# Kernel tuning notes

Measured on AMD Instinct MI355X. Metric: run time of the kernel, lower is better.

The kernel has to match this reference:

```python
import jax, jax.numpy as jnp
import numpy as np

B, S, HID = 1, 2048, 2048
NH = 16
QL, KVL = 1536, 512
DN, DR, DV = 128, 64, 128
DQ = DN + DR  # 192
IH, ID = 4, 128
TOPK = 1024
EPS = 1e-6
THETA = 10000.0


def rope_interleaved(x, cos, sin):
    # x: (b,s,h,d); cos/sin: (s,d//2); pairs are (x[...,2i], x[...,2i+1])
    xr = x[..., 0::2]
    xi = x[..., 1::2]
    c = cos[None, :, None, :]
    s = sin[None, :, None, :]
    yr = xr * c - xi * s
    yi = xr * s + xi * c
    return jnp.stack([yr, yi], axis=-1).reshape(x.shape)


def rope_noninterleaved(x, cos, sin):
    # rotate-half style: pairs are (x[...,i], x[...,i+d/2])
    d = x.shape[-1] // 2
    x1, x2 = x[..., :d], x[..., d:]
    c = cos[None, :, None, :]
    s = sin[None, :, None, :]
    return jnp.concatenate([x1 * c - x2 * s, x1 * s + x2 * c], axis=-1)


def rmsnorm(x, w):
    var = jnp.mean(x * x, axis=-1, keepdims=True)
    return w * (x * jax.lax.rsqrt(var + EPS))


def layernorm(x, g, b):
    mu = jnp.mean(x, axis=-1, keepdims=True)
    var = jnp.mean((x - mu) ** 2, axis=-1, keepdims=True)
    return (x - mu) * jax.lax.rsqrt(var + EPS) * g + b


def setup_inputs() -> dict:
    key = jax.random.key(0)
    ks = jax.random.split(key, 12)
    std = 0.02
    x = jax.random.normal(ks[0], (B, S, HID), jnp.float32)
    pos = jnp.arange(S, dtype=jnp.float32)
    inv_freq = THETA ** (-jnp.arange(0, DR, 2, dtype=jnp.float32) / DR)
    ang = pos[:, None] * inv_freq[None, :]  # (S, DR//2)
    cos, sin = jnp.cos(ang), jnp.sin(ang)
    mask = jnp.where(jnp.tril(jnp.ones((S, S), bool)), 0.0, -1e9).astype(jnp.float32)
    return {
        "x": x, "cos": cos, "sin": sin, "mask": mask,
        "Wq_a": jax.random.normal(ks[1], (HID, QL), jnp.float32) * std,
        "q_norm_w": jnp.ones((QL,), jnp.float32),
        "Wq_b": jax.random.normal(ks[2], (QL, NH * DQ), jnp.float32) * std,
        "Wkv_a": jax.random.normal(ks[3], (HID, KVL + DR), jnp.float32) * std,
        "kv_norm_w": jnp.ones((KVL,), jnp.float32),
        "Wkv_b": jax.random.normal(ks[4], (KVL, NH * (DN + DV)), jnp.float32) * std,
        "Wo": jax.random.normal(ks[5], (NH * DV, HID), jnp.float32) * std,
        "IWq_b": jax.random.normal(ks[6], (QL, IH * ID), jnp.float32) * std,
        "IWk": jax.random.normal(ks[7], (HID, ID), jnp.float32) * std,
        "Ik_norm_w": jnp.ones((ID,), jnp.float32),
        "Ik_norm_b": jnp.zeros((ID,), jnp.float32),
        "IWproj": jax.random.normal(ks[8], (HID, IH), jnp.float32) * std,
    }


def indexer(x, qr, cos, sin, mask, IWq_b, IWk, Ik_norm_w, Ik_norm_b, IWproj):
    b, s, _ = x.shape
    q = (qr @ IWq_b).reshape(b, s, IH, ID)
    q_pe, q_nope = q[..., :DR], q[..., DR:]
    q_pe = rope_noninterleaved(q_pe, cos, sin)
    q = jnp.concatenate([q_pe, q_nope], axis=-1)
    k = layernorm(x @ IWk, Ik_norm_w, Ik_norm_b)  # (b,s,ID)
    k_pe = rope_noninterleaved(k[:, :, None, :DR], cos, sin)[:, :, 0]
    k = jnp.concatenate([k_pe, k[..., DR:]], axis=-1)
    weights = (x @ IWproj) * (IH ** -0.5) * (ID ** -0.5)  # (b,s,IH)
    logits = jax.nn.relu(jnp.einsum('bthd,bsd->btsh', q, k))
    index_score = jnp.einsum('btsh,bth->bts', logits, weights)
    index_score = index_score + mask[None]
    k_top = min(TOPK, s)
    topk_idx = jax.lax.top_k(index_score, k_top)[1]  # (b,s,k)
    bi = jnp.arange(b)[:, None, None]
    si = jnp.arange(s)[None, :, None]
    index_mask = jnp.full((b, s, s), -1e9, jnp.float32).at[bi, si, topk_idx].set(0.0)
    return index_mask


def reference(x, cos, sin, mask, Wq_a, q_norm_w, Wq_b, Wkv_a, kv_norm_w, Wkv_b, Wo,
              IWq_b, IWk, Ik_norm_w, Ik_norm_b, IWproj):
    b, s, _ = x.shape
    qr = rmsnorm(x @ Wq_a, q_norm_w)  # (b,s,QL)
    q = (qr @ Wq_b).reshape(b, s, NH, DQ)
    q_nope, q_pe = q[..., :DN], q[..., DN:]
    q_pe = rope_interleaved(q_pe, cos, sin)
    q = jnp.concatenate([q_nope, q_pe], axis=-1)
    kv_full = x @ Wkv_a
    kv, k_pe = kv_full[..., :KVL], kv_full[..., KVL:]
    kv = rmsnorm(kv, kv_norm_w)
    k_pe = rope_interleaved(k_pe[:, :, None, :], cos, sin)  # (b,s,1,DR)
    kv_exp = (kv @ Wkv_b).reshape(b, s, NH, DN + DV)
    k_nope, v = kv_exp[..., :DN], kv_exp[..., DN:]
    k = jnp.concatenate([k_nope, jnp.broadcast_to(k_pe, (b, s, NH, DR))], axis=-1)
    scores = jnp.einsum('bshd,bthd->bsht', q, k) * (DQ ** -0.5)
    index_mask = indexer(x, qr, cos, sin, mask, IWq_b, IWk, Ik_norm_w, Ik_norm_b, IWproj)
    scores = scores + index_mask[:, :, None, :] + mask[None, :, None, :]
    probs = jax.nn.softmax(scores, axis=-1)
    out = jnp.einsum('bsht,bthd->bshd', probs, v).reshape(b, s, NH * DV)
    return out @ Wo
```

## Files before the change

### kernel.cpp

```cpp
#include <hip/hip_runtime.h>
#include <math.h>
#include <stdint.h>

#define S 2048
#define HID 2048
#define NH 16
#define QL 1536
#define KVL 512
#define DN 128
#define DR 64
#define DV 128
#define DQ 192
#define IH 4
#define ID 128
#define TOPK 1024

#define N1 2244
#define N2 3584

#define CDIV(a,b) (((a)+(b)-1)/(b))

typedef float f32x4 __attribute__((ext_vector_type(4)));
typedef short bf16x8 __attribute__((ext_vector_type(8)));

__device__ __forceinline__ ushort f2b(float f) {
    uint32_t u = __float_as_uint(f);
    u += 0x7fffu + ((u >> 16) & 1u);
    return (ushort)(u >> 16);
}

#define GLL16(g, l)                                                            \
    __builtin_amdgcn_global_load_lds(                                          \
        (const __attribute__((address_space(1))) void*)(g),                    \
        (__attribute__((address_space(3))) void*)(l), 16, 0, 0)

__global__ __launch_bounds__(256) void gemm_bt(const ushort* __restrict__ A,
                                               const ushort* __restrict__ BT,
                                               float* __restrict__ C,
                                               int M, int N, int K) {
    __shared__ ushort As[128 * 32];
    __shared__ ushort Bs[128 * 32];
    const int tid = threadIdx.x;
    const int w = tid >> 6, l = tid & 63;
    const int quad = l >> 4, lane = l & 15;
    const int row0 = blockIdx.y * 128, col0 = blockIdx.x * 128;
    const int wr = (w >> 1) * 64, wc = (w & 1) * 64;
    f32x4 acc[4][4];
#pragma unroll
    for (int i = 0; i < 4; i++)
#pragma unroll
        for (int j = 0; j < 4; j++) acc[i][j] = (f32x4)0.f;

    const int srow = w * 32 + (l >> 2);
    const int c8 = (l & 3) * 8;
    const ushort* pa0 = A + (size_t)(row0 + srow) * K + c8;
    const ushort* pa1 = A + (size_t)(row0 + srow + 16) * K + c8;
    int bn0 = col0 + srow;      if (bn0 > N - 1) bn0 = N - 1;
    int bn1 = col0 + srow + 16; if (bn1 > N - 1) bn1 = N - 1;
    const ushort* pb0 = BT + (size_t)bn0 * K + c8;
    const ushort* pb1 = BT + (size_t)bn1 * K + c8;
    ushort* sa0 = As + srow * 32 + c8;
    ushort* sa1 = sa0 + 16 * 32;
    ushort* sb0 = Bs + srow * 32 + c8;
    ushort* sb1 = sb0 + 16 * 32;

    for (int k0 = 0; k0 < K; k0 += 32) {
        __syncthreads();
        GLL16(pa0 + k0, sa0);
        GLL16(pa1 + k0, sa1);
        GLL16(pb0 + k0, sb0);
        GLL16(pb1 + k0, sb1);
        __syncthreads();
        bf16x8 af[4], bf[4];
#pragma unroll
        for (int mi = 0; mi < 4; mi++)
            af[mi] = *(const bf16x8*)(As + (wr + mi * 16 + lane) * 32 + quad * 8);
#pragma unroll
        for (int ni = 0; ni < 4; ni++)
            bf[ni] = *(const bf16x8*)(Bs + (wc + ni * 16 + lane) * 32 + quad * 8);
#pragma unroll
        for (int mi = 0; mi < 4; mi++)
#pragma unroll
            for (int ni = 0; ni < 4; ni++)
                acc[mi][ni] = __builtin_amdgcn_mfma_f32_16x16x32_bf16(af[mi], bf[ni], acc[mi][ni], 0, 0, 0);
    }
#pragma unroll
    for (int mi = 0; mi < 4; mi++)
#pragma unroll
        for (int ni = 0; ni < 4; ni++)
#pragma unroll
            for (int r = 0; r < 4; r++) {
                int row = row0 + wr + mi * 16 + quad * 4 + r;
                int col = col0 + wc + ni * 16 + lane;
                if (col < N) C[(size_t)row * N + col] = acc[mi][ni][r];
            }
}

__global__ __launch_bounds__(256) void gemm_bt_h(const ushort* __restrict__ A,
                                                 const ushort* __restrict__ BT,
                                                 ushort* __restrict__ C,
                                                 int M, int N, int K) {
    __shared__ ushort As[128 * 32];
    __shared__ ushort Bs[128 * 32];
    const int tid = threadIdx.x;
    const int w = tid >> 6, l = tid & 63;
    const int quad = l >> 4, lane = l & 15;
    const int row0 = blockIdx.y * 128, col0 = blockIdx.x * 128;
    const int wr = (w >> 1) * 64, wc = (w & 1) * 64;
    f32x4 acc[4][4];
#pragma unroll
    for (int i = 0; i < 4; i++)
#pragma unroll
        for (int j = 0; j < 4; j++) acc[i][j] = (f32x4)0.f;

    const int srow = w * 32 + (l >> 2);
    const int c8 = (l & 3) * 8;
    const ushort* pa0 = A + (size_t)(row0 + srow) * K + c8;
    const ushort* pa1 = A + (size_t)(row0 + srow + 16) * K + c8;
    int bn0 = col0 + srow;      if (bn0 > N - 1) bn0 = N - 1;
    int bn1 = col0 + srow + 16; if (bn1 > N - 1) bn1 = N - 1;
    const ushort* pb0 = BT + (size_t)bn0 * K + c8;
    const ushort* pb1 = BT + (size_t)bn1 * K + c8;
    ushort* sa0 = As + srow * 32 + c8;
    ushort* sa1 = sa0 + 16 * 32;
    ushort* sb0 = Bs + srow * 32 + c8;
    ushort* sb1 = sb0 + 16 * 32;

    for (int k0 = 0; k0 < K; k0 += 32) {
        __syncthreads();
        GLL16(pa0 + k0, sa0);
        GLL16(pa1 + k0, sa1);
        GLL16(pb0 + k0, sb0);
        GLL16(pb1 + k0, sb1);
        __syncthreads();
        bf16x8 af[4], bf[4];
#pragma unroll
        for (int mi = 0; mi < 4; mi++)
            af[mi] = *(const bf16x8*)(As + (wr + mi * 16 + lane) * 32 + quad * 8);
#pragma unroll
        for (int ni = 0; ni < 4; ni++)
            bf[ni] = *(const bf16x8*)(Bs + (wc + ni * 16 + lane) * 32 + quad * 8);
#pragma unroll
        for (int mi = 0; mi < 4; mi++)
#pragma unroll
            for (int ni = 0; ni < 4; ni++)
                acc[mi][ni] = __builtin_amdgcn_mfma_f32_16x16x32_bf16(af[mi], bf[ni], acc[mi][ni], 0, 0, 0);
    }
#pragma unroll
    for (int mi = 0; mi < 4; mi++)
#pragma unroll
        for (int ni = 0; ni < 4; ni++)
#pragma unroll
            for (int r = 0; r < 4; r++) {
                int row = row0 + wr + mi * 16 + quad * 4 + r;
                int col = col0 + wc + ni * 16 + lane;
                if (col < N) C[(size_t)row * N + col] = f2b(acc[mi][ni][r]);
            }
}

__global__ __launch_bounds__(256) void wtrans(const float* __restrict__ W, ushort* __restrict__ WT,
                                              int K, int N) {
    __shared__ float t[64][65];
    int k0 = blockIdx.x * 64, n0 = blockIdx.y * 64;
    int rr = threadIdx.x >> 6, cc = threadIdx.x & 63;
#pragma unroll
    for (int p = 0; p < 16; p++) {
        int k = k0 + p * 4 + rr, n = n0 + cc;
        t[p * 4 + rr][cc] = (k < K && n < N) ? W[(size_t)k * N + n] : 0.f;
    }
    __syncthreads();
#pragma unroll
    for (int p = 0; p < 16; p++) {
        int n = n0 + p * 4 + rr, k = k0 + cc;
        if (n < N && k < K) WT[(size_t)n * K + k] = f2b(t[cc][p * 4 + rr]);
    }
}

__global__ void cvt_bf16(const float* __restrict__ in, ushort* __restrict__ out) {
    int i = blockIdx.x * 256 + threadIdx.x;
    float4 v = *(const float4*)(in + (size_t)i * 4);
    uint32_t lo = (uint32_t)f2b(v.x) | ((uint32_t)f2b(v.y) << 16);
    uint32_t hi = (uint32_t)f2b(v.z) | ((uint32_t)f2b(v.w) << 16);
    *(uint2*)(out + (size_t)i * 4) = make_uint2(lo, hi);
}

__global__ __launch_bounds__(256) void rmsnorm_b(const float* __restrict__ in, int istride,
                                                 ushort* __restrict__ out, int ostride,
                                                 const float* __restrict__ w, int L) {
    int row = blockIdx.x, tid = threadIdx.x;
    const float* xr = in + (size_t)row * istride;
    ushort* yr = out + (size_t)row * ostride;
    __shared__ float red[256];
    float ss = 0.f;
    for (int i = tid; i < L; i += 256) { float v = xr[i]; ss += v * v; }
    red[tid] = ss; __syncthreads();
    for (int st = 128; st > 0; st >>= 1) {
        if (tid < st) red[tid] += red[tid + st];
        __syncthreads();
    }
    float scale = rsqrtf(red[0] / (float)L + 1e-6f);
    for (int i = tid; i < L; i += 256) yr[i] = f2b(xr[i] * scale * w[i]);
}

__global__ void rope_q_b(const float* __restrict__ qf, ushort* __restrict__ qb,
                         const float* __restrict__ cosb, const float* __restrict__ sinb) {
    int idx = blockIdx.x * 256 + threadIdx.x;
    int p = idx % 96, h = (idx / 96) & 15, t = idx / (96 * 16);
    const float sc = 0.07216878364870322f;
    const float* src = qf + (size_t)t * N2 + h * 192;
    ushort* dst = qb + ((size_t)h * S + t) * 192;
    if (p < 64) {
        dst[2 * p]     = f2b(src[2 * p] * sc);
        dst[2 * p + 1] = f2b(src[2 * p + 1] * sc);
    } else {
        int j = p - 64;
        float c = cosb[t * 32 + j], s = sinb[t * 32 + j];
        float xr = src[128 + 2 * j], xi = src[128 + 2 * j + 1];
        dst[128 + 2 * j]     = f2b((xr * c - xi * s) * sc);
        dst[128 + 2 * j + 1] = f2b((xr * s + xi * c) * sc);
    }
}

__global__ void rope_kpe_kernel(const float* __restrict__ kvf, float* __restrict__ kpe,
                                const float* __restrict__ cosb, const float* __restrict__ sinb) {
    int idx = blockIdx.x * 256 + threadIdx.x;
    int j = idx & 31, t = idx >> 5;
    float c = cosb[t * 32 + j], s = sinb[t * 32 + j];
    const float* p = kvf + (size_t)t * N1 + 2 * j;
    float xr = p[0], xi = p[1];
    kpe[t * 64 + 2 * j] = xr * c - xi * s;
    kpe[t * 64 + 2 * j + 1] = xr * s + xi * c;
}

__global__ __launch_bounds__(256) void pack_kv(const ushort* __restrict__ kvexp_h,
                                               const float* __restrict__ kpe,
                                               ushort* __restrict__ kb,
                                               ushort* __restrict__ vT) {
    __shared__ ushort t[64][136];
    const int s0 = blockIdx.x * 64, h = blockIdx.y, tid = threadIdx.x;
    const int row = tid >> 2, c = tid & 3;
    const ushort* src = kvexp_h + (size_t)(s0 + row) * 4096 + h * 256;
    ushort* kbr = kb + ((size_t)h * S + s0 + row) * 192;
#pragma unroll
    for (int i = 0; i < 4; i++) {
        int off = c * 32 + i * 8;
        *(uint4*)(kbr + off) = *(const uint4*)(src + off);
        *(uint4*)(&t[row][off]) = *(const uint4*)(src + 128 + off);
    }
    const float* kp = kpe + (size_t)(s0 + row) * 64 + c * 16;
#pragma unroll
    for (int i = 0; i < 16; i++) kbr[128 + c * 16 + i] = f2b(kp[i]);
    __syncthreads();
    const int d = tid >> 1, sh = (tid & 1) * 32;
    ushort* dst = vT + ((size_t)h * 128 + d) * S + s0 + sh;
#pragma unroll
    for (int i = 0; i < 32; i++) dst[i] = t[sh + i][d];
}

__global__ void rope_qi_kernel(float* __restrict__ qi, const float* __restrict__ cosb,
                               const float* __restrict__ sinb) {
    int idx = blockIdx.x * 256 + threadIdx.x;
    int j = idx & 31, h = (idx >> 5) & 3, t = idx >> 7;
    float c = cosb[t * 32 + j], s = sinb[t * 32 + j];
    float* p = qi + (size_t)t * N2 + h * ID;
    float x1 = p[j], x2 = p[j + 32];
    p[j] = x1 * c - x2 * s;
    p[j + 32] = x1 * s + x2 * c;
}

__global__ __launch_bounds__(128) void ki_ln_rope_kernel(float* __restrict__ ki,
                                                         const float* __restrict__ g,
                                                         const float* __restrict__ bb,
                                                         const float* __restrict__ cosb,
                                                         const float* __restrict__ sinb) {
    int t = blockIdx.x, tid = threadIdx.x;
    float* p = ki + (size_t)t * N1;
    __shared__ float s1[128], s2m[128];
    float v = p[tid];
    s1[tid] = v; s2m[tid] = v * v; __syncthreads();
    for (int st = 64; st > 0; st >>= 1) {
        if (tid < st) { s1[tid] += s1[tid + st]; s2m[tid] += s2m[tid + st]; }
        __syncthreads();
    }
    float mu = s1[0] / 128.f;
    float var = s2m[0] / 128.f - mu * mu;
    float y = (v - mu) * rsqrtf(var + 1e-6f) * g[tid] + bb[tid];
    __syncthreads();
    s1[tid] = y; __syncthreads();
    if (tid >= 64) {
        p[tid] = y;
    } else if (tid < 32) {
        float c = cosb[t * 32 + tid], s = sinb[t * 32 + tid];
        float x1 = s1[tid], x2 = s1[tid + 32];
        p[tid] = x1 * c - x2 * s;
        p[tid + 32] = x1 * s + x2 * c;
    }
}

__global__ void transpose_ki_kernel(const float* __restrict__ ki, float* __restrict__ kiT) {
    int idx = blockIdx.x * 256 + threadIdx.x;
    int t = idx >> 7, d = idx & 127;
    kiT[(size_t)d * S + t] = ki[(size_t)t * N1 + d];
}

__global__ __launch_bounds__(256) void iscore4(const float* __restrict__ qi,
                                               const float* __restrict__ kiT,
                                               const float* __restrict__ iw,
                                               float* __restrict__ iscore) {
    int t = blockIdx.x;
    int s0 = blockIdx.y * 1024;
    if (s0 > t) return;
    int s = s0 + threadIdx.x * 4;
    __shared__ float qs[4 * ID];
    __shared__ float ws4[4];
    for (int i = threadIdx.x; i < 4 * ID; i += 256) qs[i] = qi[(size_t)t * N2 + i];
    if (threadIdx.x < 4) ws4[threadIdx.x] = iw[(size_t)t * N1 + threadIdx.x] * 0.04419417382415922f;
    __syncthreads();
    if (s > t) return;
    float a[4][4];
#pragma unroll
    for (int h = 0; h < 4; h++)
#pragma unroll
        for (int c = 0; c < 4; c++) a[h][c] = 0.f;
    for (int d = 0; d < ID; d++) {
        float4 kv = *(const float4*)(kiT + (size_t)d * S + s);
#pragma unroll
        for (int h = 0; h < 4; h++) {
            float qv = qs[h * ID + d];
            a[h][0] += qv * kv.x; a[h][1] += qv * kv.y;
            a[h][2] += qv * kv.z; a[h][3] += qv * kv.w;
        }
    }
#pragma unroll
    for (int c = 0; c < 4; c++) {
        if (s + c > t) break;
        float sc = fmaxf(a[0][c], 0.f) * ws4[0] + fmaxf(a[1][c], 0.f) * ws4[1] +
                   fmaxf(a[2][c], 0.f) * ws4[2] + fmaxf(a[3][c], 0.f) * ws4[3];
        iscore[(size_t)t * S + s + c] = sc;
    }
}

__device__ inline unsigned sortable_u32(float f) {
    unsigned u = __float_as_uint(f);
    return (u & 0x80000000u) ? ~u : (u | 0x80000000u);
}

__global__ __launch_bounds__(256) void topk_mask(const float* __restrict__ iscore,
                                                 uint32_t* __restrict__ msk) {
    int t = blockIdx.x, tid = threadIdx.x;
    uint32_t* mrow = msk + (size_t)t * 64;
    if (t < TOPK) {
        if (tid < 64) {
            int full = (t + 1) >> 5;
            uint32_t wv2 = (tid < full) ? 0xFFFFFFFFu : 0u;
            if (tid == full) { int rem = (t + 1) & 31; wv2 = rem ? ((1u << rem) - 1u) : 0u; }
            mrow[tid] = wv2;
        }
        return;
    }
    const float* row = iscore + (size_t)t * S;
    const int n = t + 1;
    const int wv = tid >> 6;
    __shared__ int hist[4][256];
    __shared__ int scan[256];
    __shared__ int bsel, ksel;
    __shared__ uint32_t bytes[256];

    int jb = tid * 8;
    float4 v0 = *(const float4*)(row + jb);
    float4 v1 = *(const float4*)(row + jb + 4);
    uint32_t lsu[8];
    {
        float vvv[8] = {v0.x, v0.y, v0.z, v0.w, v1.x, v1.y, v1.z, v1.w};
#pragma unroll
        for (int i = 0; i < 8; i++)
            lsu[i] = (jb + i < n) ? sortable_u32(vvv[i]) : 0u;
    }
    unsigned prefix = 0, prefmask = 0;
    int k = TOPK;
    for (int pass = 0; pass < 4; pass++) {
        int shift = 24 - pass * 8;
#pragma unroll
        for (int r = 0; r < 4; r++) hist[r][tid] = 0;
        __syncthreads();
#pragma unroll
        for (int i = 0; i < 8; i++) {
            uint32_t u = lsu[i];
            if ((u & prefmask) == prefix) atomicAdd(&hist[wv][(u >> shift) & 255], 1);
        }
        __syncthreads();
        int h = hist[0][tid] + hist[1][tid] + hist[2][tid] + hist[3][tid];
        scan[tid] = h; __syncthreads();
        for (int st = 1; st < 256; st <<= 1) {
            int a = scan[tid];
            int b = (tid + st < 256) ? scan[tid + st] : 0;
            __syncthreads();
            scan[tid] = a + b;
            __syncthreads();
        }
        int snext = (tid < 255) ? scan[tid + 1] : 0;
        if (scan[tid] >= k && snext < k) { bsel = tid; ksel = k - snext; }
        __syncthreads();
        prefix |= ((unsigned)bsel) << shift;
        prefmask |= 0xFFu << shift;
        k = ksel;
        __syncthreads();
    }
    const unsigned u_thr = prefix;
    const int need = k;
    uint32_t gtbits = 0, eqbits = 0;
    int eqcnt = 0;
#pragma unroll
    for (int i = 0; i < 8; i++) {
        uint32_t u = lsu[i];
        if (u > u_thr) gtbits |= 1u << i;
        else if (u == u_thr) { eqbits |= 1u << i; eqcnt++; }
    }
    scan[tid] = eqcnt; __syncthreads();
    for (int st = 1; st < 256; st <<= 1) {
        int a = scan[tid];
        int b = (tid >= st) ? scan[tid - st] : 0;
        __syncthreads();
        scan[tid] = a + b;
        __syncthreads();
    }
    int room = need - (scan[tid] - eqcnt);
    uint32_t keep = 0;
#pragma unroll
    for (int i = 0; i < 8; i++)
        if ((eqbits >> i) & 1u) { if (room > 0) { keep |= 1u << i; room--; } }
    bytes[tid] = gtbits | keep;
    __syncthreads();
    if (tid < 64)
        mrow[tid] = bytes[tid * 4] | (bytes[tid * 4 + 1] << 8) |
                    (bytes[tid * 4 + 2] << 16) | (bytes[tid * 4 + 3] << 24);
}

__global__ __launch_bounds__(256, 2) void fattn4(const ushort* __restrict__ qb,
                                                 const ushort* __restrict__ kb,
                                                 const ushort* __restrict__ vT,
                                                 const uint32_t* __restrict__ msk,
                                                 float* __restrict__ Opart,
                                                 float* __restrict__ mlbuf) {
    __shared__ ushort Ks[6 * 64 * 32];
    __shared__ ushort Vs[2 * 128 * 32];
    __shared__ ushort Pm[4][16 * 72];
    const int tid = threadIdx.x;
    const int w = tid >> 6, l = tid & 63, quad = l >> 4, lane = l & 15;
    const int b = blockIdx.x;
    const int r8 = b & 7, j = b >> 3;
    const int h = r8 + 8 * (j & 1);
    const int idx = j >> 1;
    const int pair = idx & 15, part = idx >> 4;
    const int ta = pair, tb = 31 - pair, nA = ta + 1;
    const int vlo = part ? 17 : 0, vhi = part ? 33 : 17;
    const int qa0 = ta * 64, qb0 = tb * 64;

    bf16x8 qfa[6], qfb[6];
    {
        const ushort* qpa = qb + ((size_t)h * S + qa0 + w * 16 + lane) * 192;
        const ushort* qpb = qb + ((size_t)h * S + qb0 + w * 16 + lane) * 192;
#pragma unroll
        for (int ks = 0; ks < 6; ks++) {
            qfa[ks] = *(const bf16x8*)(qpa + ks * 32 + quad * 8);
            qfb[ks] = *(const bf16x8*)(qpb + ks * 32 + quad * 8);
        }
    }
    f32x4 oa[8], ob[8];
#pragma unroll
    for (int i = 0; i < 8; i++) { oa[i] = (f32x4)0.f; ob[i] = (f32x4)0.f; }
    float ma[4], la[4], mb[4], lb[4];
#pragma unroll
    for (int r = 0; r < 4; r++) { ma[r] = -1e30f; la[r] = 0.f; mb[r] = -1e30f; lb[r] = 0.f; }

    ushort* pw = &Pm[w][0];
    const ushort* kbase = kb + (size_t)h * S * 192;
    const ushort* vbase = vT + (size_t)h * 128 * S;

    for (int kt = 0; kt <= tb; kt++) {
        const int idxB = (kt <= ta) ? 2 * kt : kt + nA;
        const int hasA = (kt <= ta);
        const int idxA = 2 * kt + 1;
        const bool doB = (idxB >= vlo && idxB < vhi);
        const bool doA = hasA && (idxA >= vlo && idxA < vhi);
        if (!(doA || doB)) continue;
        const int s0 = kt * 64;
        __syncthreads();
#pragma unroll
        for (int ii = 0; ii < 6; ii++) {
            const int i = w * 6 + ii;
            const int jk = i >> 2, rb = (i & 3) << 4;
            const ushort* src = kbase + (size_t)(s0 + rb + (l >> 2)) * 192 + jk * 32 + (l & 3) * 8;
            GLL16(src, Ks + jk * 2048 + rb * 32 + l * 8);
        }
#pragma unroll
        for (int ii = 0; ii < 4; ii++) {
            const int i = w * 4 + ii;
            const int j2 = i >> 3, db = (i & 7) << 4;
            const ushort* src = vbase + (size_t)(db + (l >> 2)) * S + s0 + j2 * 32 + (l & 3) * 8;
            GLL16(src, Vs + j2 * 4096 + db * 32 + l * 8);
        }
        __syncthreads();

#pragma unroll
        for (int pass = 0; pass < 2; pass++) {
            if (pass == 0 && !doA) continue;
            if (pass == 1 && !doB) continue;
            const bf16x8* qf = (pass == 0) ? qfa : qfb;
            f32x4* oacc      = (pass == 0) ? oa : ob;
            float* mm        = (pass == 0) ? ma : mb;
            float* ll        = (pass == 0) ? la : lb;
            const int q0t    = (pass == 0) ? qa0 : qb0;

            f32x4 sc[4];
#pragma unroll
            for (int kq = 0; kq < 4; kq++) {
                sc[kq] = (f32x4)0.f;
#pragma unroll
                for (int ks = 0; ks < 6; ks++) {
                    bf16x8 bfr = *(const bf16x8*)(Ks + ks * 2048 + (kq * 16 + lane) * 32 + quad * 8);
                    sc[kq] = __builtin_amdgcn_mfma_f32_16x16x32_bf16(qf[ks], bfr, sc[kq], 0, 0, 0);
                }
            }
            uint32_t w0[4], w1[4];
            {
                const int rowbase = q0t + w * 16 + quad * 4;
#pragma unroll
                for (int r = 0; r < 4; r++) {
                    const uint32_t* mp = msk + (size_t)(rowbase + r) * 64 + (s0 >> 5);
                    w0[r] = mp[0]; w1[r] = mp[1];
                }
            }
            float vmax[4] = {-1e30f, -1e30f, -1e30f, -1e30f};
#pragma unroll
            for (int kq = 0; kq < 4; kq++) {
                const int sh = (kq & 1) * 16 + lane;
#pragma unroll
                for (int r = 0; r < 4; r++) {
                    uint32_t word = (kq < 2) ? w0[r] : w1[r];
                    float v = ((word >> sh) & 1u) ? sc[kq][r] : -1e30f;
                    sc[kq][r] = v;
                    vmax[r] = fmaxf(vmax[r], v);
                }
            }
#pragma unroll
            for (int off = 1; off < 16; off <<= 1)
#pragma unroll
                for (int r = 0; r < 4; r++)
                    vmax[r] = fmaxf(vmax[r], __shfl_xor(vmax[r], off, 64));
            float alpha[4], psum[4];
#pragma unroll
            for (int r = 0; r < 4; r++) {
                float mnew = fmaxf(mm[r], vmax[r]);
                alpha[r] = __expf(mm[r] - mnew);
                mm[r] = mnew;
                psum[r] = 0.f;
            }
#pragma unroll
            for (int kq = 0; kq < 4; kq++)
#pragma unroll
                for (int r = 0; r < 4; r++) {
                    float v = sc[kq][r];
                    float e = (v < -1e29f) ? 0.f : __expf(v - mm[r]);
                    psum[r] += e;
                    pw[(quad * 4 + r) * 72 + kq * 16 + lane] = f2b(e);
                }
#pragma unroll
            for (int off = 1; off < 16; off <<= 1)
#pragma unroll
                for (int r = 0; r < 4; r++)
                    psum[r] += __shfl_xor(psum[r], off, 64);
#pragma unroll
            for (int r = 0; r < 4; r++) ll[r] = ll[r] * alpha[r] + psum[r];

            bf16x8 pfr[2];
#pragma unroll
            for (int k2 = 0; k2 < 2; k2++)
                pfr[k2] = *(const bf16x8*)(pw + lane * 72 + k2 * 32 + quad * 8);
#pragma unroll
            for (int nt = 0; nt < 8; nt++) {
#pragma unroll
                for (int r = 0; r < 4; r++) oacc[nt][r] *= alpha[r];
#pragma unroll
                for (int k2 = 0; k2 < 2; k2++) {
                    bf16x8 vfr = *(const bf16x8*)(Vs + k2 * 4096 + (nt * 16 + lane) * 32 + quad * 8);
                    oacc[nt] = __builtin_amdgcn_mfma_f32_16x16x32_bf16(pfr[k2], vfr, oacc[nt], 0, 0, 0);
                }
            }
        }
    }
#pragma unroll
    for (int pass = 0; pass < 2; pass++) {
        const f32x4* oacc = (pass == 0) ? oa : ob;
        const float* mm   = (pass == 0) ? ma : mb;
        const float* ll   = (pass == 0) ? la : lb;
        const int qt      = (pass == 0) ? ta : tb;
        float* Op = Opart + (size_t)(((qt * 16 + h) * 2) + part) * (64 * 128);
        float* mlp = mlbuf + (size_t)(((qt * 16 + h) * 2) + part) * 128;
#pragma unroll
        for (int nt = 0; nt < 8; nt++)
#pragma unroll
            for (int r = 0; r < 4; r++)
                Op[(w * 16 + quad * 4 + r) * 128 + nt * 16 + lane] = oacc[nt][r];
        if (lane == 0) {
#pragma unroll
            for (int r = 0; r < 4; r++) {
                mlp[(w * 16 + quad * 4 + r) * 2 + 0] = mm[r];
                mlp[(w * 16 + quad * 4 + r) * 2 + 1] = ll[r];
            }
        }
    }
}

__global__ __launch_bounds__(256) void attn_combine(const float* __restrict__ Opart,
                                                    const float* __restrict__ mlbuf,
                                                    ushort* __restrict__ attn_b) {
    const int qt = blockIdx.x, h = blockIdx.y, tid = threadIdx.x;
    const size_t base = ((size_t)qt * 16 + h) * 2;
    const float* Op0 = Opart + base * (64 * 128);
    const float* Op1 = Op0 + 64 * 128;
    const float* ml0 = mlbuf + base * 128;
    const float* ml1 = ml0 + 128;
#pragma unroll
    for (int i = 0; i < 32; i++) {
        int id = tid + i * 256;
        int row = id >> 7, d = id & 127;
        float m0 = ml0[row * 2], l0 = ml0[row * 2 + 1];
        float m1 = ml1[row * 2], l1 = ml1[row * 2 + 1];
        float m = fmaxf(m0, m1);
        float e0 = __expf(m0 - m), e1 = __expf(m1 - m);
        float linv = 1.f / (l0 * e0 + l1 * e1);
        float v = (Op0[id] * e0 + Op1[id] * e1) * linv;
        attn_b[(size_t)(qt * 64 + row) * 2048 + h * 128 + d] = f2b(v);
    }
}

extern "C" void kernel_launch(void* const* d_in, const int* in_sizes, int n_in,
                              void* d_out, int out_size, void* d_ws, size_t ws_size,
                              hipStream_t stream) {
    const float* x        = (const float*)d_in[0];
    const float* cosb     = (const float*)d_in[1];
    const float* sinb     = (const float*)d_in[2];
    const float* Wq_a     = (const float*)d_in[4];
    const float* q_norm_w = (const float*)d_in[5];
    const float* Wq_b     = (const float*)d_in[6];
    const float* Wkv_a    = (const float*)d_in[7];
    const float* kv_norm_w= (const float*)d_in[8];
    const float* Wkv_b    = (const float*)d_in[9];
    const float* Wo       = (const float*)d_in[10];
    const float* IWq_b    = (const float*)d_in[11];
    const float* IWk      = (const float*)d_in[12];
    const float* Ik_norm_w= (const float*)d_in[13];
    const float* Ik_norm_b= (const float*)d_in[14];
    const float* IWproj   = (const float*)d_in[15];
    float* out = (float*)d_out;

    char* ws = (char*)d_ws;
    size_t o = 0;
    auto take = [&](size_t b) { char* p = ws + o; o += (b + 255) & ~(size_t)255; return p; };
    ushort* xb     = (ushort*)take((size_t)S * HID * 2);
    ushort* qrb    = (ushort*)take((size_t)S * QL * 2);
    ushort* qb     = (ushort*)take((size_t)NH * S * DQ * 2);
    ushort* kvnb   = (ushort*)take((size_t)S * KVL * 2);
    float*  kpe    = (float*)take((size_t)S * DR * 4);
    ushort* kb     = (ushort*)take((size_t)NH * S * DQ * 2);
    ushort* vT     = (ushort*)take((size_t)NH * DV * S * 2);
    uint32_t* msk  = (uint32_t*)take((size_t)S * 64 * 4);
    float*  mlbuf  = (float*)take((size_t)32 * 16 * 2 * 64 * 2 * 4);
    ushort* WTp    = (ushort*)take((size_t)N2 * QL * 2);
    float*  C1     = (float*)take((size_t)S * N1 * 4);
    char*   big    = take((size_t)S * 4096 * 4 + 1024);
    ushort* kvexp_h= (ushort*)take((size_t)S * 4096 * 2);
    float*  kiT    = (float*)take((size_t)128 * S * 4);
    char*   poolb  = take((size_t)16777216);

    float* C2     = (float*)big;
    float* Opart  = (float*)big;
    float* iscore = (float*)poolb;
    ushort* attn_b = (ushort*)poolb;

    cvt_bf16<<<(S * HID) / 1024, 256, 0, stream>>>(x, xb);

    wtrans<<<dim3(32, 24), 256, 0, stream>>>(Wq_a, WTp, HID, QL);
    wtrans<<<dim3(32, 9),  256, 0, stream>>>(Wkv_a, WTp + (size_t)1536 * HID, HID, KVL + DR);
    wtrans<<<dim3(32, 2),  256, 0, stream>>>(IWk, WTp + (size_t)2112 * HID, HID, ID);
    wtrans<<<dim3(32, 1),  256, 0, stream>>>(IWproj, WTp + (size_t)2240 * HID, HID, IH);
    gemm_bt<<<dim3(CDIV(N1, 128), S / 128), 256, 0, stream>>>(xb, WTp, C1, S, N1, HID);

    rmsnorm_b<<<S, 256, 0, stream>>>(C1, N1, qrb, QL, q_norm_w, QL);
    rmsnorm_b<<<S, 256, 0, stream>>>(C1 + 1536, N1, kvnb, KVL, kv_norm_w, KVL);
    rope_kpe_kernel<<<(S * 32) / 256, 256, 0, stream>>>(C1 + 2048, kpe, cosb, sinb);
    ki_ln_rope_kernel<<<S, 128, 0, stream>>>(C1 + 2112, Ik_norm_w, Ik_norm_b, cosb, sinb);
    transpose_ki_kernel<<<(S * ID) / 256, 256, 0, stream>>>(C1 + 2112, kiT);

    wtrans<<<dim3(24, 48), 256, 0, stream>>>(Wq_b, WTp, QL, NH * DQ);
    wtrans<<<dim3(24, 8),  256, 0, stream>>>(IWq_b, WTp + (size_t)3072 * QL, QL, IH * ID);
    gemm_bt<<<dim3(N2 / 128, S / 128), 256, 0, stream>>>(qrb, WTp, C2, S, N2, QL);
    rope_q_b<<<(S * NH * 96) / 256, 256, 0, stream>>>(C2, qb, cosb, sinb);
    rope_qi_kernel<<<(S * IH * 32) / 256, 256, 0, stream>>>(C2 + 3072, cosb, sinb);

    wtrans<<<dim3(8, 64), 256, 0, stream>>>(Wkv_b, WTp, KVL, NH * (DN + DV));
    gemm_bt_h<<<dim3(32, S / 128), 256, 0, stream>>>(kvnb, WTp, kvexp_h, S, NH * (DN + DV), KVL);
    pack_kv<<<dim3(S / 64, NH), 256, 0, stream>>>(kvexp_h, kpe, kb, vT);

    iscore4<<<dim3(S, S / 1024), 256, 0, stream>>>(C2 + 3072, kiT, C1 + 2240, iscore);
    topk_mask<<<S, 256, 0, stream>>>(iscore, msk);

    fattn4<<<512, 256, 0, stream>>>(qb, kb, vT, msk, Opart, mlbuf);
    attn_combine<<<dim3(32, 16), 256, 0, stream>>>(Opart, mlbuf, attn_b);

    wtrans<<<dim3(32, 32), 256, 0, stream>>>(Wo, WTp, NH * DV, HID);
    gemm_bt<<<dim3(HID / 128, S / 128), 256, 0, stream>>>(attn_b, WTp, out, S, HID, NH * DV);

    (void)in_sizes; (void)n_in; (void)out_size; (void)ws_size; (void)o;
}
```

Baseline: 551.7 us.

## Fuse pre/post-GEMM elementwise kernels and split attention KV range three ways

Merges the weight-transpose launches into two multi-weight kernels and fuses the rmsnorm, rope, layernorm and transpose passes that follow each projection GEMM into single per-row kernels, cutting launch count and repeated passes over C1/C2. The flash-attention kernel now splits each query tile's KV range into three parts instead of two, with 768 blocks and a 3-wave occupancy bound, and the combine step merges three partials. LDS tiles are relaid out so each MFMA fragment reads contiguous 16-byte chunks. Softmax switches to exp2 with the log2(e) factor folded into the query scale. The extra partial buffer adds memory traffic, and the fused per-row kernels serialize several reductions behind block barriers.

```diff
diff --git a/kernel.cpp b/kernel.cpp
--- a/kernel.cpp
+++ b/kernel.cpp
@@ -158,10 +158,9 @@
             }
 }
 
-__global__ __launch_bounds__(256) void wtrans(const float* __restrict__ W, ushort* __restrict__ WT,
-                                              int K, int N) {
+__device__ __forceinline__ void wtrans_body(const float* W, ushort* WT, int K, int N,
+                                            int k0, int n0) {
     __shared__ float t[64][65];
-    int k0 = blockIdx.x * 64, n0 = blockIdx.y * 64;
     int rr = threadIdx.x >> 6, cc = threadIdx.x & 63;
 #pragma unroll
     for (int p = 0; p < 16; p++) {
@@ -174,6 +173,32 @@
         int n = n0 + p * 4 + rr, k = k0 + cc;
         if (n < N && k < K) WT[(size_t)n * K + k] = f2b(t[cc][p * 4 + rr]);
     }
+}
+
+__global__ __launch_bounds__(256) void wtrans(const float* __restrict__ W, ushort* __restrict__ WT,
+                                              int K, int N) {
+    wtrans_body(W, WT, K, N, blockIdx.x * 64, blockIdx.y * 64);
+}
+
+__global__ __launch_bounds__(256) void wtrans_c1(const float* __restrict__ W0, const float* __restrict__ W1,
+                                                 const float* __restrict__ W2, const float* __restrict__ W3,
+                                                 ushort* __restrict__ WT) {
+    int yb = blockIdx.y;
+    const float* W; int N; size_t off; int y;
+    if (yb < 24)      { W = W0; N = 1536; off = 0;                      y = yb; }
+    else if (yb < 33) { W = W1; N = 576;  off = (size_t)1536 * HID;     y = yb - 24; }
+    else if (yb < 35) { W = W2; N = 128;  off = (size_t)2112 * HID;     y = yb - 33; }
+    else              { W = W3; N = 4;    off = (size_t)2240 * HID;     y = yb - 35; }
+    wtrans_body(W, WT + off, HID, N, blockIdx.x * 64, y * 64);
+}
+
+__global__ __launch_bounds__(256) void wtrans_c2(const float* __restrict__ W0, const float* __restrict__ W1,
+                                                 ushort* __restrict__ WT) {
+    int yb = blockIdx.y;
+    const float* W; int N; size_t off; int y;
+    if (yb < 48) { W = W0; N = 3072; off = 0;                  y = yb; }
+    else         { W = W1; N = 512;  off = (size_t)3072 * QL;  y = yb - 48; }
+    wtrans_body(W, WT + off, QL, N, blockIdx.x * 64, y * 64);
 }
 
 __global__ void cvt_bf16(const float* __restrict__ in, ushort* __restrict__ out) {
@@ -184,52 +209,100 @@
     *(uint2*)(out + (size_t)i * 4) = make_uint2(lo, hi);
 }
 
-__global__ __launch_bounds__(256) void rmsnorm_b(const float* __restrict__ in, int istride,
-                                                 ushort* __restrict__ out, int ostride,
-                                                 const float* __restrict__ w, int L) {
-    int row = blockIdx.x, tid = threadIdx.x;
-    const float* xr = in + (size_t)row * istride;
-    ushort* yr = out + (size_t)row * ostride;
+__global__ __launch_bounds__(256) void post_c1(const float* __restrict__ C1,
+                                               const float* __restrict__ qw,
+                                               const float* __restrict__ kvw,
+                                               const float* __restrict__ ikg,
+                                               const float* __restrict__ ikb,
+                                               const float* __restrict__ cosb,
+                                               const float* __restrict__ sinb,
+                                               ushort* __restrict__ qrb,
+                                               ushort* __restrict__ kvnb,
+                                               float* __restrict__ kpe,
+                                               float* __restrict__ kiT) {
+    const int t = blockIdx.x, tid = threadIdx.x;
+    const float* row = C1 + (size_t)t * N1;
     __shared__ float red[256];
+    __shared__ float kis[128];
     float ss = 0.f;
-    for (int i = tid; i < L; i += 256) { float v = xr[i]; ss += v * v; }
+    for (int i = tid; i < 1536; i += 256) { float v = row[i]; ss += v * v; }
     red[tid] = ss; __syncthreads();
-    for (int st = 128; st > 0; st >>= 1) {
-        if (tid < st) red[tid] += red[tid + st];
-        __syncthreads();
-    }
-    float scale = rsqrtf(red[0] / (float)L + 1e-6f);
-    for (int i = tid; i < L; i += 256) yr[i] = f2b(xr[i] * scale * w[i]);
-}
-
-__global__ void rope_q_b(const float* __restrict__ qf, ushort* __restrict__ qb,
-                         const float* __restrict__ cosb, const float* __restrict__ sinb) {
-    int idx = blockIdx.x * 256 + threadIdx.x;
-    int p = idx % 96, h = (idx / 96) & 15, t = idx / (96 * 16);
-    const float sc = 0.07216878364870322f;
-    const float* src = qf + (size_t)t * N2 + h * 192;
-    ushort* dst = qb + ((size_t)h * S + t) * 192;
-    if (p < 64) {
-        dst[2 * p]     = f2b(src[2 * p] * sc);
-        dst[2 * p + 1] = f2b(src[2 * p + 1] * sc);
-    } else {
-        int j = p - 64;
-        float c = cosb[t * 32 + j], s = sinb[t * 32 + j];
-        float xr = src[128 + 2 * j], xi = src[128 + 2 * j + 1];
-        dst[128 + 2 * j]     = f2b((xr * c - xi * s) * sc);
-        dst[128 + 2 * j + 1] = f2b((xr * s + xi * c) * sc);
-    }
-}
-
-__global__ void rope_kpe_kernel(const float* __restrict__ kvf, float* __restrict__ kpe,
-                                const float* __restrict__ cosb, const float* __restrict__ sinb) {
-    int idx = blockIdx.x * 256 + threadIdx.x;
-    int j = idx & 31, t = idx >> 5;
-    float c = cosb[t * 32 + j], s = sinb[t * 32 + j];
-    const float* p = kvf + (size_t)t * N1 + 2 * j;
-    float xr = p[0], xi = p[1];
-    kpe[t * 64 + 2 * j] = xr * c - xi * s;
-    kpe[t * 64 + 2 * j + 1] = xr * s + xi * c;
+    for (int st = 128; st > 0; st >>= 1) { if (tid < st) red[tid] += red[tid + st]; __syncthreads(); }
+    float sq = rsqrtf(red[0] / 1536.f + 1e-6f);
+    __syncthreads();
+    float s2 = 0.f;
+    for (int i = tid; i < 512; i += 256) { float v = row[1536 + i]; s2 += v * v; }
+    red[tid] = s2; __syncthreads();
+    for (int st = 128; st > 0; st >>= 1) { if (tid < st) red[tid] += red[tid + st]; __syncthreads(); }
+    float skv = rsqrtf(red[0] / 512.f + 1e-6f);
+    __syncthreads();
+    float kv_ = (tid < 128) ? row[2112 + tid] : 0.f;
+    red[tid] = kv_; __syncthreads();
+    for (int st = 128; st > 0; st >>= 1) { if (tid < st) red[tid] += red[tid + st]; __syncthreads(); }
+    float mu = red[0] / 128.f;
+    __syncthreads();
+    red[tid] = kv_ * kv_; __syncthreads();
+    for (int st = 128; st > 0; st >>= 1) { if (tid < st) red[tid] += red[tid + st]; __syncthreads(); }
+    float var = red[0] / 128.f - mu * mu;
+    for (int i = tid; i < 1536; i += 256) qrb[(size_t)t * QL + i] = f2b(row[i] * sq * qw[i]);
+    for (int i = tid; i < 512; i += 256)  kvnb[(size_t)t * KVL + i] = f2b(row[1536 + i] * skv * kvw[i]);
+    if (tid < 32) {
+        float c = cosb[t * 32 + tid], s = sinb[t * 32 + tid];
+        float xr = row[2048 + 2 * tid], xi = row[2048 + 2 * tid + 1];
+        kpe[t * 64 + 2 * tid]     = xr * c - xi * s;
+        kpe[t * 64 + 2 * tid + 1] = xr * s + xi * c;
+    }
+    if (tid < 128) kis[tid] = (kv_ - mu) * rsqrtf(var + 1e-6f) * ikg[tid] + ikb[tid];
+    __syncthreads();
+    if (tid < 128) {
+        float outv;
+        if (tid < 32) {
+            float c = cosb[t * 32 + tid], s = sinb[t * 32 + tid];
+            outv = kis[tid] * c - kis[tid + 32] * s;
+        } else if (tid < 64) {
+            int j = tid - 32;
+            float c = cosb[t * 32 + j], s = sinb[t * 32 + j];
+            outv = kis[j] * s + kis[tid] * c;
+        } else {
+            outv = kis[tid];
+        }
+        kiT[(size_t)tid * S + t] = outv;
+    }
+}
+
+__global__ __launch_bounds__(256) void post_c2(float* __restrict__ C2,
+                                               const float* __restrict__ cosb,
+                                               const float* __restrict__ sinb,
+                                               ushort* __restrict__ qb) {
+    const int t = blockIdx.x, tid = threadIdx.x;
+    __shared__ float cs[32], sn[32];
+    if (tid < 32) { cs[tid] = cosb[t * 32 + tid]; sn[tid] = sinb[t * 32 + tid]; }
+    __syncthreads();
+    const float sc = 0.10412775370051047f;
+    const float* src0 = C2 + (size_t)t * N2;
+    for (int i = tid; i < NH * 96; i += 256) {
+        int h = i / 96, p = i % 96;
+        const float* src = src0 + h * 192;
+        ushort* dst = qb + ((size_t)h * S + t) * 192;
+        if (p < 64) {
+            dst[2 * p]     = f2b(src[2 * p] * sc);
+            dst[2 * p + 1] = f2b(src[2 * p + 1] * sc);
+        } else {
+            int j = p - 64;
+            float c = cs[j], s = sn[j];
+            float xr = src[128 + 2 * j], xi = src[128 + 2 * j + 1];
+            dst[128 + 2 * j]     = f2b((xr * c - xi * s) * sc);
+            dst[128 + 2 * j + 1] = f2b((xr * s + xi * c) * sc);
+        }
+    }
+    if (tid < 128) {
+        int h = tid >> 5, j = tid & 31;
+        float* p = C2 + (size_t)t * N2 + 3072 + h * 128;
+        float c = cs[j], s = sn[j];
+        float x1 = p[j], x2 = p[j + 32];
+        p[j] = x1 * c - x2 * s;
+        p[j + 32] = x1 * s + x2 * c;
+    }
 }
 
 __global__ __launch_bounds__(256) void pack_kv(const ushort* __restrict__ kvexp_h,
@@ -255,52 +328,6 @@
     ushort* dst = vT + ((size_t)h * 128 + d) * S + s0 + sh;
 #pragma unroll
     for (int i = 0; i < 32; i++) dst[i] = t[sh + i][d];
-}
-
-__global__ void rope_qi_kernel(float* __restrict__ qi, const float* __restrict__ cosb,
-                               const float* __restrict__ sinb) {
-    int idx = blockIdx.x * 256 + threadIdx.x;
-    int j = idx & 31, h = (idx >> 5) & 3, t = idx >> 7;
-    float c = cosb[t * 32 + j], s = sinb[t * 32 + j];
-    float* p = qi + (size_t)t * N2 + h * ID;
-    float x1 = p[j], x2 = p[j + 32];
-    p[j] = x1 * c - x2 * s;
-    p[j + 32] = x1 * s + x2 * c;
-}
-
-__global__ __launch_bounds__(128) void ki_ln_rope_kernel(float* __restrict__ ki,
-                                                         const float* __restrict__ g,
-                                                         const float* __restrict__ bb,
-                                                         const float* __restrict__ cosb,
-                                                         const float* __restrict__ sinb) {
-    int t = blockIdx.x, tid = threadIdx.x;
-    float* p = ki + (size_t)t * N1;
-    __shared__ float s1[128], s2m[128];
-    float v = p[tid];
-    s1[tid] = v; s2m[tid] = v * v; __syncthreads();
-    for (int st = 64; st > 0; st >>= 1) {
-        if (tid < st) { s1[tid] += s1[tid + st]; s2m[tid] += s2m[tid + st]; }
-        __syncthreads();
-    }
-    float mu = s1[0] / 128.f;
-    float var = s2m[0] / 128.f - mu * mu;
-    float y = (v - mu) * rsqrtf(var + 1e-6f) * g[tid] + bb[tid];
-    __syncthreads();
-    s1[tid] = y; __syncthreads();
-    if (tid >= 64) {
-        p[tid] = y;
-    } else if (tid < 32) {
-        float c = cosb[t * 32 + tid], s = sinb[t * 32 + tid];
-        float x1 = s1[tid], x2 = s1[tid + 32];
-        p[tid] = x1 * c - x2 * s;
-        p[tid + 32] = x1 * s + x2 * c;
-    }
-}
-
-__global__ void transpose_ki_kernel(const float* __restrict__ ki, float* __restrict__ kiT) {
-    int idx = blockIdx.x * 256 + threadIdx.x;
-    int t = idx >> 7, d = idx & 127;
-    kiT[(size_t)d * S + t] = ki[(size_t)t * N1 + d];
 }
 
 __global__ __launch_bounds__(256) void iscore4(const float* __restrict__ qi,
@@ -436,14 +463,14 @@
                     (bytes[tid * 4 + 2] << 16) | (bytes[tid * 4 + 3] << 24);
 }
 
-__global__ __launch_bounds__(256, 2) void fattn4(const ushort* __restrict__ qb,
+__global__ __launch_bounds__(256, 3) void fattn5(const ushort* __restrict__ qb,
                                                  const ushort* __restrict__ kb,
                                                  const ushort* __restrict__ vT,
                                                  const uint32_t* __restrict__ msk,
                                                  float* __restrict__ Opart,
                                                  float* __restrict__ mlbuf) {
-    __shared__ ushort Ks[6 * 64 * 32];
-    __shared__ ushort Vs[2 * 128 * 32];
+    __shared__ ushort Ks[24 * 512];
+    __shared__ ushort Vs[16 * 512];
     __shared__ ushort Pm[4][16 * 72];
     const int tid = threadIdx.x;
     const int w = tid >> 6, l = tid & 63, quad = l >> 4, lane = l & 15;
@@ -453,7 +480,7 @@
     const int idx = j >> 1;
     const int pair = idx & 15, part = idx >> 4;
     const int ta = pair, tb = 31 - pair, nA = ta + 1;
-    const int vlo = part ? 17 : 0, vhi = part ? 33 : 17;
+    const int vlo = part * 11, vhi = vlo + 11;
     const int qa0 = ta * 64, qb0 = tb * 64;
 
     bf16x8 qfa[6], qfb[6];
@@ -489,16 +516,16 @@
 #pragma unroll
         for (int ii = 0; ii < 6; ii++) {
             const int i = w * 6 + ii;
-            const int jk = i >> 2, rb = (i & 3) << 4;
-            const ushort* src = kbase + (size_t)(s0 + rb + (l >> 2)) * 192 + jk * 32 + (l & 3) * 8;
-            GLL16(src, Ks + jk * 2048 + rb * 32 + l * 8);
+            const int ks = i >> 2, kq = i & 3;
+            const ushort* src = kbase + (size_t)(s0 + kq * 16 + lane) * 192 + ks * 32 + quad * 8;
+            GLL16(src, Ks + i * 512 + l * 8);
         }
 #pragma unroll
         for (int ii = 0; ii < 4; ii++) {
             const int i = w * 4 + ii;
-            const int j2 = i >> 3, db = (i & 7) << 4;
-            const ushort* src = vbase + (size_t)(db + (l >> 2)) * S + s0 + j2 * 32 + (l & 3) * 8;
-            GLL16(src, Vs + j2 * 4096 + db * 32 + l * 8);
+            const int k2 = i >> 3, nt = i & 7;
+            const ushort* src = vbase + (size_t)(nt * 16 + lane) * S + s0 + k2 * 32 + quad * 8;
+            GLL16(src, Vs + i * 512 + l * 8);
         }
         __syncthreads();
 
@@ -518,7 +545,7 @@
                 sc[kq] = (f32x4)0.f;
 #pragma unroll
                 for (int ks = 0; ks < 6; ks++) {
-                    bf16x8 bfr = *(const bf16x8*)(Ks + ks * 2048 + (kq * 16 + lane) * 32 + quad * 8);
+                    bf16x8 bfr = *(const bf16x8*)(Ks + (ks * 4 + kq) * 512 + quad * 128 + lane * 8);
                     sc[kq] = __builtin_amdgcn_mfma_f32_16x16x32_bf16(qf[ks], bfr, sc[kq], 0, 0, 0);
                 }
             }
@@ -552,7 +579,7 @@
 #pragma unroll
             for (int r = 0; r < 4; r++) {
                 float mnew = fmaxf(mm[r], vmax[r]);
-                alpha[r] = __expf(mm[r] - mnew);
+                alpha[r] = exp2f(mm[r] - mnew);
                 mm[r] = mnew;
                 psum[r] = 0.f;
             }
@@ -561,7 +588,7 @@
 #pragma unroll
                 for (int r = 0; r < 4; r++) {
                     float v = sc[kq][r];
-                    float e = (v < -1e29f) ? 0.f : __expf(v - mm[r]);
+                    float e = (v < -1e29f) ? 0.f : exp2f(v - mm[r]);
                     psum[r] += e;
                     pw[(quad * 4 + r) * 72 + kq * 16 + lane] = f2b(e);
                 }
@@ -583,7 +610,7 @@
                 for (int r = 0; r < 4; r++) oacc[nt][r] *= alpha[r];
 #pragma unroll
                 for (int k2 = 0; k2 < 2; k2++) {
-                    bf16x8 vfr = *(const bf16x8*)(Vs + k2 * 4096 + (nt * 16 + lane) * 32 + quad * 8);
+                    bf16x8 vfr = *(const bf16x8*)(Vs + ((k2 * 8 + nt) * 4 + quad) * 128 + lane * 8);
                     oacc[nt] = __builtin_amdgcn_mfma_f32_16x16x32_bf16(pfr[k2], vfr, oacc[nt], 0, 0, 0);
                 }
             }
@@ -595,8 +622,8 @@
         const float* mm   = (pass == 0) ? ma : mb;
         const float* ll   = (pass == 0) ? la : lb;
         const int qt      = (pass == 0) ? ta : tb;
-        float* Op = Opart + (size_t)(((qt * 16 + h) * 2) + part) * (64 * 128);
-        float* mlp = mlbuf + (size_t)(((qt * 16 + h) * 2) + part) * 128;
+        float* Op = Opart + (size_t)((qt * 16 + h) * 3 + part) * (64 * 128);
+        float* mlp = mlbuf + (size_t)((qt * 16 + h) * 3 + part) * 128;
 #pragma unroll
         for (int nt = 0; nt < 8; nt++)
 #pragma unroll
@@ -616,21 +643,24 @@
                                                     const float* __restrict__ mlbuf,
                                                     ushort* __restrict__ attn_b) {
     const int qt = blockIdx.x, h = blockIdx.y, tid = threadIdx.x;
-    const size_t base = ((size_t)qt * 16 + h) * 2;
-    const float* Op0 = Opart + base * (64 * 128);
-    const float* Op1 = Op0 + 64 * 128;
+    const size_t base = ((size_t)qt * 16 + h) * 3;
+    const float* Op0 = Opart + base * 8192;
+    const float* Op1 = Op0 + 8192;
+    const float* Op2 = Op1 + 8192;
     const float* ml0 = mlbuf + base * 128;
     const float* ml1 = ml0 + 128;
+    const float* ml2 = ml1 + 128;
 #pragma unroll
     for (int i = 0; i < 32; i++) {
         int id = tid + i * 256;
         int row = id >> 7, d = id & 127;
         float m0 = ml0[row * 2], l0 = ml0[row * 2 + 1];
         float m1 = ml1[row * 2], l1 = ml1[row * 2 + 1];
-        float m = fmaxf(m0, m1);
-        float e0 = __expf(m0 - m), e1 = __expf(m1 - m);
-        float linv = 1.f / (l0 * e0 + l1 * e1);
-        float v = (Op0[id] * e0 + Op1[id] * e1) * linv;
+        float m2 = ml2[row * 2], l2 = ml2[row * 2 + 1];
+        float m = fmaxf(fmaxf(m0, m1), m2);
+        float e0 = exp2f(m0 - m), e1 = exp2f(m1 - m), e2 = exp2f(m2 - m);
+        float linv = 1.f / (l0 * e0 + l1 * e1 + l2 * e2);
+        float v = (Op0[id] * e0 + Op1[id] * e1 + Op2[id] * e2) * linv;
         attn_b[(size_t)(qt * 64 + row) * 2048 + h * 128 + d] = f2b(v);
     }
 }
@@ -666,10 +696,10 @@
     ushort* kb     = (ushort*)take((size_t)NH * S * DQ * 2);
     ushort* vT     = (ushort*)take((size_t)NH * DV * S * 2);
     uint32_t* msk  = (uint32_t*)take((size_t)S * 64 * 4);
-    float*  mlbuf  = (float*)take((size_t)32 * 16 * 2 * 64 * 2 * 4);
+    float*  mlbuf  = (float*)take((size_t)32 * 16 * 3 * 64 * 2 * 4);
     ushort* WTp    = (ushort*)take((size_t)N2 * QL * 2);
     float*  C1     = (float*)take((size_t)S * N1 * 4);
-    char*   big    = take((size_t)S * 4096 * 4 + 1024);
+    char*   big    = take((size_t)32 * 16 * 3 * 8192 * 4 + 1024);
     ushort* kvexp_h= (ushort*)take((size_t)S * 4096 * 2);
     float*  kiT    = (float*)take((size_t)128 * S * 4);
     char*   poolb  = take((size_t)16777216);
@@ -681,23 +711,14 @@
 
     cvt_bf16<<<(S * HID) / 1024, 256, 0, stream>>>(x, xb);
 
-    wtrans<<<dim3(32, 24), 256, 0, stream>>>(Wq_a, WTp, HID, QL);
-    wtrans<<<dim3(32, 9),  256, 0, stream>>>(Wkv_a, WTp + (size_t)1536 * HID, HID, KVL + DR);
-    wtrans<<<dim3(32, 2),  256, 0, stream>>>(IWk, WTp + (size_t)2112 * HID, HID, ID);
-    wtrans<<<dim3(32, 1),  256, 0, stream>>>(IWproj, WTp + (size_t)2240 * HID, HID, IH);
+    wtrans_c1<<<dim3(32, 36), 256, 0, stream>>>(Wq_a, Wkv_a, IWk, IWproj, WTp);
     gemm_bt<<<dim3(CDIV(N1, 128), S / 128), 256, 0, stream>>>(xb, WTp, C1, S, N1, HID);
-
-    rmsnorm_b<<<S, 256, 0, stream>>>(C1, N1, qrb, QL, q_norm_w, QL);
-    rmsnorm_b<<<S, 256, 0, stream>>>(C1 + 1536, N1, kvnb, KVL, kv_norm_w, KVL);
-    rope_kpe_kernel<<<(S * 32) / 256, 256, 0, stream>>>(C1 + 2048, kpe, cosb, sinb);
-    ki_ln_rope_kernel<<<S, 128, 0, stream>>>(C1 + 2112, Ik_norm_w, Ik_norm_b, cosb, sinb);
-    transpose_ki_kernel<<<(S * ID) / 256, 256, 0, stream>>>(C1 + 2112, kiT);
-
-    wtrans<<<dim3(24, 48), 256, 0, stream>>>(Wq_b, WTp, QL, NH * DQ);
-    wtrans<<<dim3(24, 8),  256, 0, stream>>>(IWq_b, WTp + (size_t)3072 * QL, QL, IH * ID);
+    post_c1<<<S, 256, 0, stream>>>(C1, q_norm_w, kv_norm_w, Ik_norm_w, Ik_norm_b,
+                                   cosb, sinb, qrb, kvnb, kpe, kiT);
+
+    wtrans_c2<<<dim3(24, 56), 256, 0, stream>>>(Wq_b, IWq_b, WTp);
     gemm_bt<<<dim3(N2 / 128, S / 128), 256, 0, stream>>>(qrb, WTp, C2, S, N2, QL);
-    rope_q_b<<<(S * NH * 96) / 256, 256, 0, stream>>>(C2, qb, cosb, sinb);
-    rope_qi_kernel<<<(S * IH * 32) / 256, 256, 0, stream>>>(C2 + 3072, cosb, sinb);
+    post_c2<<<S, 256, 0, stream>>>(C2, cosb, sinb, qb);
 
     wtrans<<<dim3(8, 64), 256, 0, stream>>>(Wkv_b, WTp, KVL, NH * (DN + DV));
     gemm_bt_h<<<dim3(32, S / 128), 256, 0, stream>>>(kvnb, WTp, kvexp_h, S, NH * (DN + DV), KVL);
@@ -706,7 +727,7 @@
     iscore4<<<dim3(S, S / 1024), 256, 0, stream>>>(C2 + 3072, kiT, C1 + 2240, iscore);
     topk_mask<<<S, 256, 0, stream>>>(iscore, msk);
 
-    fattn4<<<512, 256, 0, stream>>>(qb, kb, vT, msk, Opart, mlbuf);
+    fattn5<<<768, 256, 0, stream>>>(qb, kb, vT, msk, Opart, mlbuf);
     attn_combine<<<dim3(32, 16), 256, 0, stream>>>(Opart, mlbuf, attn_b);
 
     wtrans<<<dim3(32, 32), 256, 0, stream>>>(Wo, WTp, NH * DV, HID);
```

After: 570.1 us. +3.3%, slower.
